# Optimization experiments

Measured on AMD Instinct MI355X. Metric: run time of the kernel, lower is better.

## Reference

```python
import jax, jax.numpy as jnp
import numpy as np

B, S, IN, D, H, FF, L = 16, 1000, 32, 512, 8, 2048, 6
DK = D // H
EPS = 1e-5


def setup_inputs() -> dict:
    key = jax.random.key(0)
    ks = iter(jax.random.split(key, 64))
    def w(shape, s=0.02):
        return jax.random.normal(next(ks), shape, dtype=jnp.float32) * s
    inp = {
        'x': jax.random.normal(next(ks), (B, S, IN), dtype=jnp.float32),
        # input projection
        'Win': w((IN, D)), 'b_in': jnp.zeros((D,), jnp.float32),
        # per-layer attention weights (stacked over L layers)
        'Wq': w((L, D, D)), 'bq': jnp.zeros((L, D), jnp.float32),
        'Wk': w((L, D, D)), 'bk': jnp.zeros((L, D), jnp.float32),
        'Wv': w((L, D, D)), 'bv': jnp.zeros((L, D), jnp.float32),
        'Wo': w((L, D, D)), 'bo': jnp.zeros((L, D), jnp.float32),
        # per-layer feed-forward
        'W1': w((L, D, FF)), 'b1': jnp.zeros((L, FF), jnp.float32),
        'W2': w((L, FF, D)), 'b2': jnp.zeros((L, D), jnp.float32),
        # per-layer layernorms
        'ln1_g': jnp.ones((L, D), jnp.float32), 'ln1_b': jnp.zeros((L, D), jnp.float32),
        'ln2_g': jnp.ones((L, D), jnp.float32), 'ln2_b': jnp.zeros((L, D), jnp.float32),
        # final encoder norm
        'lnf_g': jnp.ones((D,), jnp.float32), 'lnf_b': jnp.zeros((D,), jnp.float32),
        # feature extraction head: D -> D/2 -> D/4
        'Wf1': w((D, D // 2)), 'bf1': jnp.zeros((D // 2,), jnp.float32),
        'Wf2': w((D // 2, D // 4)), 'bf2': jnp.zeros((D // 4,), jnp.float32),
        # reconstruction head: D/4 -> D/2 -> D -> IN
        'Wr1': w((D // 4, D // 2)), 'br1': jnp.zeros((D // 2,), jnp.float32),
        'Wr2': w((D // 2, D)), 'br2': jnp.zeros((D,), jnp.float32),
        'Wr3': w((D, IN)), 'br3': jnp.zeros((IN,), jnp.float32),
        # anomaly head: D/4 -> D/8 -> 1
        'Wa1': w((D // 4, D // 8)), 'ba1': jnp.zeros((D // 8,), jnp.float32),
        'Wa2': w((D // 8, 1)), 'ba2': jnp.zeros((1,), jnp.float32),
    }
    return inp


def _layernorm(x, g, b):
    m = jnp.mean(x, axis=-1, keepdims=True)
    v = jnp.var(x, axis=-1, keepdims=True)
    return (x - m) * jax.lax.rsqrt(v + EPS) * g + b


def _pos_encoding(seq_len, d_model):
    pos = jnp.arange(seq_len, dtype=jnp.float32)[:, None]
    div = jnp.exp(jnp.arange(0, d_model, 2, dtype=jnp.float32) * (-np.log(10000.0) / d_model))
    pe = jnp.zeros((seq_len, d_model), jnp.float32)
    pe = pe.at[:, 0::2].set(jnp.sin(pos * div))
    pe = pe.at[:, 1::2].set(jnp.cos(pos * div))
    return pe


def _encoder(h, Wq, bq, Wk, bk, Wv, bv, Wo, bo, W1, b1, W2, b2,
             ln1_g, ln1_b, ln2_g, ln2_b, lnf_g, lnf_b):
    h = h + _pos_encoding(h.shape[1], D)[None]
    scale = 1.0 / np.sqrt(DK)
    for i in range(L):
        # multi-head self-attention
        q = (h @ Wq[i] + bq[i]).reshape(B, S, H, DK).transpose(0, 2, 1, 3)
        k = (h @ Wk[i] + bk[i]).reshape(B, S, H, DK).transpose(0, 2, 1, 3)
        v = (h @ Wv[i] + bv[i]).reshape(B, S, H, DK).transpose(0, 2, 1, 3)
        scores = jnp.einsum('bhsd,bhtd->bhst', q, k) * scale  # [B,H,S,S]
        attn = jax.nn.softmax(scores, axis=-1)
        ctx = jnp.einsum('bhst,bhtd->bhsd', attn, v)
        ctx = ctx.transpose(0, 2, 1, 3).reshape(B, S, D)
        attn_out = ctx @ Wo[i] + bo[i]
        h = _layernorm(h + attn_out, ln1_g[i], ln1_b[i])
        # feed-forward
        ff = jax.nn.relu(h @ W1[i] + b1[i]) @ W2[i] + b2[i]
        h = _layernorm(h + ff, ln2_g[i], ln2_b[i])
    return _layernorm(h, lnf_g, lnf_b)


def reference(x, Win, b_in, Wq, bq, Wk, bk, Wv, bv, Wo, bo, W1, b1, W2, b2,
              ln1_g, ln1_b, ln2_g, ln2_b, lnf_g, lnf_b,
              Wf1, bf1, Wf2, bf2, Wr1, br1, Wr2, br2, Wr3, br3,
              Wa1, ba1, Wa2, ba2):
    h = x @ Win + b_in  # [B,S,D]
    h = _encoder(h, Wq, bq, Wk, bk, Wv, bv, Wo, bo, W1, b1, W2, b2,
                 ln1_g, ln1_b, ln2_g, ln2_b, lnf_g, lnf_b)
    feat = jax.nn.relu(h @ Wf1 + bf1) @ Wf2 + bf2  # [B,S,D/4]
    recon = jax.nn.relu(jax.nn.relu(feat @ Wr1 + br1) @ Wr2 + br2) @ Wr3 + br3  # [B,S,IN]
    anomaly = jax.nn.sigmoid(jax.nn.relu(feat @ Wa1 + ba1) @ Wa2 + ba2)  # [B,S,1]
    return recon, anomaly
```

## Files before the change

kernel.cpp:

```cpp
#include <hip/hip_runtime.h>
#include <hip/hip_bf16.h>
#include <math.h>

#define B_  16
#define S_  1000
#define IN_ 32
#define D_  512
#define H_  8
#define FF_ 2048
#define L_  6
#define DK_ 64
#define M_  (B_ * S_)
#define SP_ 1024

typedef __bf16 bf16x8 __attribute__((ext_vector_type(8)));
typedef float  floatx4 __attribute__((ext_vector_type(4)));

#define FLAG_RELU 1
#define FLAG_BF16 2
#define FLAG_QKV  4

#define QSCALE 0.18033688011112042f

__device__ __forceinline__ void gll16(const __bf16* g, __bf16* l) {
    __builtin_amdgcn_global_load_lds(
        (const __attribute__((address_space(1))) unsigned int*)g,
        (__attribute__((address_space(3))) unsigned int*)l, 16, 0, 0);
}

__global__ __launch_bounds__(256) void gemm_mfma(
    const __bf16* __restrict__ A, const __bf16* __restrict__ BT,
    const float* __restrict__ bias, void* __restrict__ C,
    int M, int N, int K, int flags)
{
    __shared__ __bf16 Asm[128 * 32];
    __shared__ __bf16 Bsm[128 * 32];

    int tid  = threadIdx.x;
    int wave = tid >> 6;
    int lane = tid & 63;
    int bm = blockIdx.y * 128;
    int bn = blockIdx.x * 128;
    int wm = (wave & 1) * 64;
    int wn = (wave >> 1) * 64;
    int lm = lane & 15;
    int lq = lane >> 4;

    floatx4 acc[4][4] = {};

    int crow  = tid >> 2;
    int cpart = (tid & 3) * 8;
    const __bf16* ag0 = A + (size_t)(bm + crow) * K + cpart;
    const __bf16* ag1 = A + (size_t)(bm + 64 + crow) * K + cpart;
    __bf16* al0 = Asm + tid * 8;
    __bf16* al1 = Asm + 2048 + tid * 8;
    int nr0 = bn + crow, nr1 = bn + 64 + crow;
    const __bf16* bg0 = BT + (size_t)nr0 * K + cpart;
    const __bf16* bg1 = BT + (size_t)nr1 * K + cpart;
    __bf16* bl0 = Bsm + tid * 8;
    __bf16* bl1 = Bsm + 2048 + tid * 8;
    bool bv0 = nr0 < N, bv1 = nr1 < N;

    for (int k0 = 0; k0 < K; k0 += 32) {
        __syncthreads();
        gll16(ag0 + k0, al0);
        gll16(ag1 + k0, al1);
        if (bv0) gll16(bg0 + k0, bl0);
        if (bv1) gll16(bg1 + k0, bl1);
        __syncthreads();

        bf16x8 af[4], bf[4];
        #pragma unroll
        for (int i = 0; i < 4; ++i) {
            af[i] = *(const bf16x8*)&Asm[(wm + i * 16 + lm) * 32 + lq * 8];
            bf[i] = *(const bf16x8*)&Bsm[(wn + i * 16 + lm) * 32 + lq * 8];
        }
        #pragma unroll
        for (int i = 0; i < 4; ++i)
            #pragma unroll
            for (int j = 0; j < 4; ++j)
                acc[i][j] = __builtin_amdgcn_mfma_f32_16x16x32_bf16(
                    af[i], bf[j], acc[i][j], 0, 0, 0);
    }

    if (flags & FLAG_QKV) {
        int sec = bn >> 9;
        if (sec < 2) {
            __bf16* dst = (__bf16*)C + (sec ? (size_t)8192000 : 0);
            #pragma unroll
            for (int j = 0; j < 4; ++j) {
                int col = (bn & 511) + wn + j * 16 + lm;
                float bvv = bias[bn + wn + j * 16 + lm];
                #pragma unroll
                for (int i = 0; i < 4; ++i)
                    #pragma unroll
                    for (int r = 0; r < 4; ++r) {
                        int m = bm + wm + i * 16 + lq * 4 + r;
                        dst[(size_t)m * 512 + col] = (__bf16)(acc[i][j][r] + bvv);
                    }
            }
        } else {
            __bf16* vt = (__bf16*)C + (size_t)16384000;
            int bbq[4], s0[4];
            #pragma unroll
            for (int i = 0; i < 4; ++i) {
                int m0 = bm + wm + i * 16 + lq * 4;
                bbq[i] = m0 / 1000;
                s0[i]  = m0 - bbq[i] * 1000;
            }
            #pragma unroll
            for (int j = 0; j < 4; ++j) {
                int col = (bn & 511) + wn + j * 16 + lm;
                float bvv = bias[bn + wn + j * 16 + lm];
                int head = col >> 6, dk = col & 63;
                #pragma unroll
                for (int i = 0; i < 4; ++i) {
                    __bf16 t4[4];
                    #pragma unroll
                    for (int r = 0; r < 4; ++r) t4[r] = (__bf16)(acc[i][j][r] + bvv);
                    *(uint2*)(vt + ((size_t)(bbq[i] * H_ + head) * DK_ + dk) * SP_ + s0[i])
                        = *(uint2*)t4;
                }
            }
        }
        return;
    }

    #pragma unroll
    for (int j = 0; j < 4; ++j) {
        int n = bn + wn + j * 16 + lm;
        if (n >= N) continue;
        float bv = bias[n];
        #pragma unroll
        for (int i = 0; i < 4; ++i) {
            #pragma unroll
            for (int r = 0; r < 4; ++r) {
                int m = bm + wm + i * 16 + lq * 4 + r;
                float v = acc[i][j][r] + bv;
                if (flags & FLAG_RELU) v = fmaxf(v, 0.f);
                if (flags & FLAG_BF16) ((__bf16*)C)[(size_t)m * N + n] = (__bf16)v;
                else                   ((float*)C)[(size_t)m * N + n] = v;
            }
        }
    }
}

__device__ __forceinline__ void trans_tile(
    const float* __restrict__ src, __bf16* __restrict__ dst,
    int K, int N, float scale, int tx0, int ty0)
{
    __shared__ float t[32][33];
    int n0 = tx0 * 32, k0 = ty0 * 32;
    int tx = threadIdx.x & 31, ty = threadIdx.x >> 5;
    #pragma unroll
    for (int i = 0; i < 32; i += 8) {
        int k = k0 + ty + i, n = n0 + tx;
        t[ty + i][tx] = (k < K && n < N) ? src[(size_t)k * N + n] * scale : 0.f;
    }
    __syncthreads();
    #pragma unroll
    for (int i = 0; i < 32; i += 8) {
        int n = n0 + ty + i, k = k0 + tx;
        if (n < N && k < K) dst[(size_t)n * K + k] = (__bf16)t[tx][ty + i];
    }
}

__global__ __launch_bounds__(256) void transpose_qkvo(
    const float* __restrict__ Wq, const float* __restrict__ Wk,
    const float* __restrict__ Wv, const float* __restrict__ Wo,
    __bf16* __restrict__ WqkvT, __bf16* __restrict__ WoT)
{
    int l = blockIdx.z >> 2, which = blockIdx.z & 3;
    const float* src; __bf16* dst; float sc = 1.f;
    size_t so = (size_t)l * 512 * 512;
    if (which == 0)      { src = Wq + so; dst = WqkvT + (size_t)l * 1536 * 512; sc = QSCALE; }
    else if (which == 1) { src = Wk + so; dst = WqkvT + (size_t)l * 1536 * 512 + 512 * 512; }
    else if (which == 2) { src = Wv + so; dst = WqkvT + (size_t)l * 1536 * 512 + 1024 * 512; }
    else                 { src = Wo + so; dst = WoT + so; }
    trans_tile(src, dst, 512, 512, sc, blockIdx.x, blockIdx.y);
}

__global__ __launch_bounds__(256) void transpose_ffn(
    const float* __restrict__ W1, const float* __restrict__ W2,
    __bf16* __restrict__ W1T, __bf16* __restrict__ W2T)
{
    int l = blockIdx.z >> 1, which = blockIdx.z & 1;
    size_t so = (size_t)l * 512 * 2048;
    int K = which ? 2048 : 512, N = which ? 512 : 2048;
    if ((int)blockIdx.x >= N / 32 || (int)blockIdx.y >= K / 32) return;
    trans_tile((which ? W2 : W1) + so, (which ? W2T : W1T) + so,
               K, N, 1.f, blockIdx.x, blockIdx.y);
}

struct TDesc { const float* src; __bf16* dst; int K; int N; float scale; };
struct TDescArr { TDesc d[7]; };

__global__ __launch_bounds__(256) void transpose_misc(TDescArr ds)
{
    TDesc t = ds.d[blockIdx.z];
    if ((int)blockIdx.x * 32 >= t.N || (int)blockIdx.y * 32 >= t.K) return;
    trans_tile(t.src, t.dst, t.K, t.N, t.scale, blockIdx.x, blockIdx.y);
}

__global__ void cast_bf16(const float* __restrict__ src, __bf16* __restrict__ dst, int n)
{
    int i = blockIdx.x * 256 + threadIdx.x;
    if (i < n) dst[i] = (__bf16)src[i];
}

__global__ void concat_bias(const float* __restrict__ bq, const float* __restrict__ bk,
                            const float* __restrict__ bv, float* __restrict__ dst)
{
    int i = blockIdx.x * 256 + threadIdx.x;
    if (i >= L_ * 1536) return;
    int l = i / 1536, j = i - l * 1536;
    float v = (j < 512) ? bq[l * 512 + j] * QSCALE
            : (j < 1024) ? bk[l * 512 + j - 512]
                         : bv[l * 512 + j - 1024];
    dst[i] = v;
}

__global__ void add_pos_kernel(float* __restrict__ h, __bf16* __restrict__ hb)
{
    int idx = blockIdx.x * 256 + threadIdx.x;
    if (idx >= B_ * S_ * D_) return;
    int d = idx % D_;
    int s = (idx / D_) % S_;
    int two_i = d & ~1;
    float ang = (float)s * expf((float)two_i * (-9.210340371976184f / (float)D_));
    float v = h[idx] + ((d & 1) ? cosf(ang) : sinf(ang));
    h[idx] = v;
    hb[idx] = (__bf16)v;
}

#define AST 72

__global__ __launch_bounds__(256) void attn_mfma(
    const __bf16* __restrict__ q, const __bf16* __restrict__ k,
    const __bf16* __restrict__ vt, __bf16* __restrict__ ctx)
{
    const int qt = blockIdx.x, hh = blockIdx.y, bb = blockIdx.z;
    const int tid = threadIdx.x;
    const int wave = tid >> 6, lane = tid & 63;
    const int lm = lane & 15, lq = lane >> 4;

    __shared__ __bf16 Ks[64 * AST];
    __shared__ __bf16 Vt[64 * AST];

    const size_t headbase = (size_t)bb * S_ * D_ + hh * DK_;
    const __bf16* kbase  = k + headbase;
    const __bf16* vtbase = vt + (size_t)(bb * H_ + hh) * DK_ * SP_;

    bf16x8 af[2][2] = {};
    #pragma unroll
    for (int iq = 0; iq < 2; ++iq) {
        int qrow = qt * 128 + wave * 32 + iq * 16 + lm;
        if (qrow < S_) {
            const __bf16* qp = q + headbase + (size_t)qrow * D_;
            af[iq][0] = *(const bf16x8*)(qp + lq * 8);
            af[iq][1] = *(const bf16x8*)(qp + 32 + lq * 8);
        }
    }

    float lsum[2] = {};
    floatx4 oacc[2][4] = {};

    const int sr  = tid >> 3;
    const int sc8 = (tid & 7) * 8;
    const int colA = (sc8 & 32) | ((sc8 & 8) << 1) | ((sc8 & 16) >> 2);

    uint4 ku[2], vu[2];
    #pragma unroll
    for (int i = 0; i < 2; ++i) {
        int r = sr + i * 32;
        ku[i] = *(const uint4*)(kbase + (size_t)r * D_ + sc8);
        vu[i] = *(const uint4*)(vtbase + (size_t)r * SP_ + sc8);
    }

    for (int jt = 0; jt < 16; ++jt) {
        const int t0 = jt * 64;
        const bool tail = (jt == 15);

        __syncthreads();
        #pragma unroll
        for (int i = 0; i < 2; ++i) {
            int r = sr + i * 32;
            *(uint4*)&Ks[r * AST + sc8] = ku[i];
            uint2 vlo = make_uint2(vu[i].x, vu[i].y);
            uint2 vhi = make_uint2(vu[i].z, vu[i].w);
            *(uint2*)&Vt[r * AST + colA]     = vlo;
            *(uint2*)&Vt[r * AST + colA + 8] = vhi;
        }
        __syncthreads();

        if (jt < 15) {
            int t0n = t0 + 64;
            #pragma unroll
            for (int i = 0; i < 2; ++i) {
                int r = sr + i * 32;
                int trow = t0n + r;
                ku[i] = (trow < S_) ? *(const uint4*)(kbase + (size_t)trow * D_ + sc8)
                                    : make_uint4(0, 0, 0, 0);
                vu[i] = *(const uint4*)(vtbase + (size_t)r * SP_ + t0n + sc8);
            }
        }

        #pragma unroll
        for (int iq = 0; iq < 2; ++iq) {
            floatx4 sacc[4] = {};
            #pragma unroll
            for (int ks = 0; ks < 2; ++ks)
                #pragma unroll
                for (int jb = 0; jb < 4; ++jb) {
                    bf16x8 kf = *(const bf16x8*)&Ks[(jb * 16 + lm) * AST + ks * 32 + lq * 8];
                    sacc[jb] = __builtin_amdgcn_mfma_f32_16x16x32_bf16(
                        kf, af[iq][ks], sacc[jb], 0, 0, 0);
                }

            __bf16 pb[4][4];
            if (!tail) {
                #pragma unroll
                for (int jb = 0; jb < 4; ++jb)
                    #pragma unroll
                    for (int r = 0; r < 4; ++r) {
                        float p = exp2f(sacc[jb][r]);
                        lsum[iq] += p;
                        pb[jb][r] = (__bf16)p;
                    }
            } else {
                #pragma unroll
                for (int jb = 0; jb < 4; ++jb)
                    #pragma unroll
                    for (int r = 0; r < 4; ++r) {
                        bool valid = (t0 + jb * 16 + lq * 4 + r) < S_;
                        float p = valid ? exp2f(sacc[jb][r]) : 0.f;
                        lsum[iq] += p;
                        pb[jb][r] = (__bf16)p;
                    }
            }

            #pragma unroll
            for (int ks = 0; ks < 2; ++ks) {
                bf16x8 pa;
                #pragma unroll
                for (int j = 0; j < 8; ++j)
                    pa[j] = pb[2 * ks + (j >> 2)][j & 3];
                #pragma unroll
                for (int jb = 0; jb < 4; ++jb) {
                    bf16x8 bv = *(const bf16x8*)&Vt[(jb * 16 + lm) * AST + ks * 32 + lq * 8];
                    oacc[iq][jb] = __builtin_amdgcn_mfma_f32_16x16x32_bf16(
                        pa, bv, oacc[iq][jb], 0, 0, 0);
                }
            }
        }
    }

    #pragma unroll
    for (int iq = 0; iq < 2; ++iq) {
        float l = lsum[iq];
        l += __shfl_xor(l, 16, 64);
        l += __shfl_xor(l, 32, 64);
        float linv[4];
        #pragma unroll
        for (int r = 0; r < 4; ++r)
            linv[r] = 1.f / __shfl(l, lq * 4 + r, 64);
        #pragma unroll
        for (int jb = 0; jb < 4; ++jb)
            #pragma unroll
            for (int r = 0; r < 4; ++r) {
                int srow = qt * 128 + wave * 32 + iq * 16 + lq * 4 + r;
                if (srow < S_)
                    ctx[headbase + (size_t)srow * D_ + jb * 16 + lm] =
                        (__bf16)(oacc[iq][jb][r] * linv[r]);
            }
    }
}

__global__ __launch_bounds__(256) void ln_kernel(
    const float* __restrict__ x, const __bf16* __restrict__ delta,
    const float* __restrict__ g, const float* __restrict__ b,
    float* __restrict__ out, __bf16* __restrict__ outb, int has_delta)
{
    int row = blockIdx.x;
    int tid = threadIdx.x;
    __shared__ float red[256];

    const size_t base = (size_t)row * D_;
    float v0 = x[base + tid];
    float v1 = x[base + tid + 256];
    if (has_delta) {
        v0 += (float)delta[base + tid];
        v1 += (float)delta[base + tid + 256];
    }
    red[tid] = v0 + v1; __syncthreads();
    for (int o = 128; o > 0; o >>= 1) {
        if (tid < o) red[tid] += red[tid + o];
        __syncthreads();
    }
    float mean = red[0] * (1.f / D_);
    __syncthreads();
    float d0 = v0 - mean, d1 = v1 - mean;
    red[tid] = d0 * d0 + d1 * d1; __syncthreads();
    for (int o = 128; o > 0; o >>= 1) {
        if (tid < o) red[tid] += red[tid + o];
        __syncthreads();
    }
    float rstd = rsqrtf(red[0] * (1.f / D_) + 1e-5f);
    float o0 = d0 * rstd * g[tid]       + b[tid];
    float o1 = d1 * rstd * g[tid + 256] + b[tid + 256];
    out[base + tid]        = o0;
    out[base + tid + 256]  = o1;
    outb[base + tid]       = (__bf16)o0;
    outb[base + tid + 256] = (__bf16)o1;
}

__global__ __launch_bounds__(256) void a2_kernel(
    const float* __restrict__ a1, const float* __restrict__ Wa2,
    const float* __restrict__ ba2, float* __restrict__ out)
{
    int row = blockIdx.x * 4 + (threadIdx.x >> 6);
    int lane = threadIdx.x & 63;
    if (row >= M_) return;
    float p = a1[(size_t)row * 64 + lane] * Wa2[lane];
    for (int o = 32; o > 0; o >>= 1) p += __shfl_down(p, o, 64);
    if (lane == 0) out[row] = 1.f / (1.f + expf(-(p + ba2[0])));
}

extern "C" void kernel_launch(void* const* d_in, const int* in_sizes, int n_in,
                              void* d_out, int out_size, void* d_ws, size_t ws_size,
                              hipStream_t stream)
{
    const float* x     = (const float*)d_in[0];
    const float* Win   = (const float*)d_in[1];
    const float* b_in  = (const float*)d_in[2];
    const float* Wq    = (const float*)d_in[3];
    const float* bq    = (const float*)d_in[4];
    const float* Wk    = (const float*)d_in[5];
    const float* bk    = (const float*)d_in[6];
    const float* Wv    = (const float*)d_in[7];
    const float* bv    = (const float*)d_in[8];
    const float* Wo    = (const float*)d_in[9];
    const float* bo    = (const float*)d_in[10];
    const float* W1    = (const float*)d_in[11];
    const float* b1    = (const float*)d_in[12];
    const float* W2    = (const float*)d_in[13];
    const float* b2    = (const float*)d_in[14];
    const float* ln1_g = (const float*)d_in[15];
    const float* ln1_b = (const float*)d_in[16];
    const float* ln2_g = (const float*)d_in[17];
    const float* ln2_b = (const float*)d_in[18];
    const float* lnf_g = (const float*)d_in[19];
    const float* lnf_b = (const float*)d_in[20];
    const float* Wf1   = (const float*)d_in[21];
    const float* bf1   = (const float*)d_in[22];
    const float* Wf2   = (const float*)d_in[23];
    const float* bf2   = (const float*)d_in[24];
    const float* Wr1   = (const float*)d_in[25];
    const float* br1   = (const float*)d_in[26];
    const float* Wr2   = (const float*)d_in[27];
    const float* br2   = (const float*)d_in[28];
    const float* Wr3   = (const float*)d_in[29];
    const float* br3   = (const float*)d_in[30];
    const float* Wa1   = (const float*)d_in[31];
    const float* ba1   = (const float*)d_in[32];
    const float* Wa2   = (const float*)d_in[33];
    const float* ba2   = (const float*)d_in[34];

    float* recon_out   = (float*)d_out;
    float* anomaly_out = (float*)d_out + (size_t)M_ * IN_;

    char* ws = (char*)d_ws;
    float*  h    = (float*)(ws + 0);
    __bf16* tmpb = (__bf16*)(ws + 32768000);
    __bf16* hb   = (__bf16*)(ws + 65536000);
    __bf16* qb   = (__bf16*)(ws + 81920000);
    __bf16* kb   = (__bf16*)(ws + 98304000);
    __bf16* vtb  = (__bf16*)(ws + 114688000);
    __bf16* ctxb = (__bf16*)(ws + 131465216);
    __bf16* ffmid = qb;

    __bf16* t1b   = (__bf16*)(ws + 81920000);
    __bf16* featb = (__bf16*)(ws + 90112000);
    __bf16* r1b   = (__bf16*)(ws + 94208000);
    __bf16* r2b   = (__bf16*)(ws + 102400000);
    float*  a1b   = (float*)(ws + 118784000);

    size_t woff = 147849216;
    auto alloc_bf = [&](size_t elems) { __bf16* p = (__bf16*)(ws + woff); woff += elems * 2; return p; };
    __bf16* WinT  = alloc_bf(32 * 512);
    __bf16* WqkvT = alloc_bf((size_t)L_ * 1536 * 512);
    __bf16* WoT   = alloc_bf((size_t)L_ * 512 * 512);
    __bf16* W1T   = alloc_bf((size_t)L_ * 512 * 2048);
    __bf16* W2T   = alloc_bf((size_t)L_ * 2048 * 512);
    __bf16* Wf1T  = alloc_bf(512 * 256);
    __bf16* Wf2T  = alloc_bf(256 * 128);
    __bf16* Wr1T  = alloc_bf(128 * 256);
    __bf16* Wr2T  = alloc_bf(256 * 512);
    __bf16* Wr3T  = alloc_bf(512 * 32);
    __bf16* Wa1T  = alloc_bf(128 * 64);
    __bf16* xb    = alloc_bf((size_t)M_ * IN_);
    float*  bqkv  = (float*)(ws + woff);  woff += (size_t)L_ * 1536 * 4;

    dim3 blk(256);
    auto gg = [](int N) { return dim3((N + 127) / 128, M_ / 128); };

    hipLaunchKernelGGL(transpose_qkvo, dim3(16, 16, L_ * 4), blk, 0, stream,
                       Wq, Wk, Wv, Wo, WqkvT, WoT);
    hipLaunchKernelGGL(transpose_ffn, dim3(64, 64, L_ * 2), blk, 0, stream,
                       W1, W2, W1T, W2T);
    TDescArr misc;
    misc.d[0] = {Win, WinT, 32, 512, 1.f};
    misc.d[1] = {Wf1, Wf1T, 512, 256, 1.f};
    misc.d[2] = {Wf2, Wf2T, 256, 128, 1.f};
    misc.d[3] = {Wr1, Wr1T, 128, 256, 1.f};
    misc.d[4] = {Wr2, Wr2T, 256, 512, 1.f};
    misc.d[5] = {Wr3, Wr3T, 512, 32, 1.f};
    misc.d[6] = {Wa1, Wa1T, 128, 64, 1.f};
    hipLaunchKernelGGL(transpose_misc, dim3(16, 16, 7), blk, 0, stream, misc);
    hipLaunchKernelGGL(cast_bf16, dim3((M_ * IN_ + 255) / 256), blk, 0, stream,
                       x, xb, M_ * IN_);
    hipLaunchKernelGGL(concat_bias, dim3((L_ * 1536 + 255) / 256), blk, 0, stream,
                       bq, bk, bv, bqkv);

    hipLaunchKernelGGL(gemm_mfma, gg(D_), blk, 0, stream,
                       xb, WinT, b_in, (void*)h, M_, D_, IN_, 0);
    hipLaunchKernelGGL(add_pos_kernel, dim3((B_ * S_ * D_ + 255) / 256), blk, 0, stream,
                       h, hb);

    for (int l = 0; l < L_; ++l) {
        size_t wo = (size_t)l * 512 * 512;
        size_t fo = (size_t)l * 512 * 2048;

        hipLaunchKernelGGL(gemm_mfma, dim3(12, M_ / 128), blk, 0, stream,
                           hb, WqkvT + (size_t)l * 1536 * 512, bqkv + (size_t)l * 1536,
                           (void*)qb, M_, 1536, 512, FLAG_QKV);

        hipLaunchKernelGGL(attn_mfma, dim3(8, H_, B_), blk, 0, stream,
                           qb, kb, vtb, ctxb);

        hipLaunchKernelGGL(gemm_mfma, gg(D_), blk, 0, stream,
                           ctxb, WoT + wo, bo + (size_t)l * D_, (void*)tmpb, M_, D_, D_,
                           FLAG_BF16);
        hipLaunchKernelGGL(ln_kernel, dim3(M_), blk, 0, stream,
                           h, tmpb, ln1_g + (size_t)l * D_, ln1_b + (size_t)l * D_, h, hb, 1);

        hipLaunchKernelGGL(gemm_mfma, gg(FF_), blk, 0, stream,
                           hb, W1T + fo, b1 + (size_t)l * FF_, (void*)ffmid, M_, FF_, D_,
                           FLAG_RELU | FLAG_BF16);
        hipLaunchKernelGGL(gemm_mfma, gg(D_), blk, 0, stream,
                           ffmid, W2T + fo, b2 + (size_t)l * D_, (void*)tmpb, M_, D_, FF_,
                           FLAG_BF16);
        hipLaunchKernelGGL(ln_kernel, dim3(M_), blk, 0, stream,
                           h, tmpb, ln2_g + (size_t)l * D_, ln2_b + (size_t)l * D_, h, hb, 1);
    }

    hipLaunchKernelGGL(ln_kernel, dim3(M_), blk, 0, stream,
                       h, nullptr, lnf_g, lnf_b, h, hb, 0);

    hipLaunchKernelGGL(gemm_mfma, gg(256), blk, 0, stream,
                       hb, Wf1T, bf1, (void*)t1b, M_, 256, 512, FLAG_RELU | FLAG_BF16);
    hipLaunchKernelGGL(gemm_mfma, gg(128), blk, 0, stream,
                       t1b, Wf2T, bf2, (void*)featb, M_, 128, 256, FLAG_BF16);

    hipLaunchKernelGGL(gemm_mfma, gg(256), blk, 0, stream,
                       featb, Wr1T, br1, (void*)r1b, M_, 256, 128, FLAG_RELU | FLAG_BF16);
    hipLaunchKernelGGL(gemm_mfma, gg(512), blk, 0, stream,
                       r1b, Wr2T, br2, (void*)r2b, M_, 512, 256, FLAG_RELU | FLAG_BF16);
    hipLaunchKernelGGL(gemm_mfma, gg(IN_), blk, 0, stream,
                       r2b, Wr3T, br3, (void*)recon_out, M_, IN_, 512, 0);

    hipLaunchKernelGGL(gemm_mfma, gg(64), blk, 0, stream,
                       featb, Wa1T, ba1, (void*)a1b, M_, 64, 128, FLAG_RELU);
    hipLaunchKernelGGL(a2_kernel, dim3((M_ + 3) / 4), blk, 0, stream,
                       a1b, Wa2, ba2, anomaly_out);
}
```

Before: 2.015 ms.

## Load attention K/V fragments directly from global memory, dropping LDS staging

The attention kernel no longer stages K and V tiles through shared memory with barriers. Each wave now loads its MFMA fragments straight from global memory, relying on the cache for reuse across the four waves of a block. Blocks are launched on a 1D grid with a remapped index so that blocks sharing a head are spread across the chip, and s_setprio wraps the MFMA bursts. Occupancy is raised through launch bounds. This removes LDS traffic and synchronisation, but every wave now issues redundant global loads and the V loads are narrow, uncoalesced 8-byte reads.

```diff
diff --git a/kernel.cpp b/kernel.cpp
--- a/kernel.cpp
+++ b/kernel.cpp
@@ -233,19 +233,17 @@
     hb[idx] = (__bf16)v;
 }
 
-#define AST 72
-
-__global__ __launch_bounds__(256) void attn_mfma(
+__global__ __launch_bounds__(256, 4) void attn_mfma(
     const __bf16* __restrict__ q, const __bf16* __restrict__ k,
     const __bf16* __restrict__ vt, __bf16* __restrict__ ctx)
 {
-    const int qt = blockIdx.x, hh = blockIdx.y, bb = blockIdx.z;
+    const int id = blockIdx.x;
+    const int w  = (id & 7) * 128 + (id >> 3);
+    const int qt = w & 7, hh = (w >> 3) & 7, bb = w >> 6;
+
     const int tid = threadIdx.x;
     const int wave = tid >> 6, lane = tid & 63;
     const int lm = lane & 15, lq = lane >> 4;
-
-    __shared__ __bf16 Ks[64 * AST];
-    __shared__ __bf16 Vt[64 * AST];
 
     const size_t headbase = (size_t)bb * S_ * D_ + hh * DK_;
     const __bf16* kbase  = k + headbase;
@@ -265,67 +263,44 @@
     float lsum[2] = {};
     floatx4 oacc[2][4] = {};
 
-    const int sr  = tid >> 3;
-    const int sc8 = (tid & 7) * 8;
-    const int colA = (sc8 & 32) | ((sc8 & 8) << 1) | ((sc8 & 16) >> 2);
-
-    uint4 ku[2], vu[2];
-    #pragma unroll
-    for (int i = 0; i < 2; ++i) {
-        int r = sr + i * 32;
-        ku[i] = *(const uint4*)(kbase + (size_t)r * D_ + sc8);
-        vu[i] = *(const uint4*)(vtbase + (size_t)r * SP_ + sc8);
-    }
+    const __bf16* kf_p = kbase  + (size_t)lm * D_  + lq * 8;
+    const __bf16* bv_p = vtbase + (size_t)lm * SP_ + lq * 4;
 
     for (int jt = 0; jt < 16; ++jt) {
         const int t0 = jt * 64;
         const bool tail = (jt == 15);
 
-        __syncthreads();
-        #pragma unroll
-        for (int i = 0; i < 2; ++i) {
-            int r = sr + i * 32;
-            *(uint4*)&Ks[r * AST + sc8] = ku[i];
-            uint2 vlo = make_uint2(vu[i].x, vu[i].y);
-            uint2 vhi = make_uint2(vu[i].z, vu[i].w);
-            *(uint2*)&Vt[r * AST + colA]     = vlo;
-            *(uint2*)&Vt[r * AST + colA + 8] = vhi;
-        }
-        __syncthreads();
-
-        if (jt < 15) {
-            int t0n = t0 + 64;
-            #pragma unroll
-            for (int i = 0; i < 2; ++i) {
-                int r = sr + i * 32;
-                int trow = t0n + r;
-                ku[i] = (trow < S_) ? *(const uint4*)(kbase + (size_t)trow * D_ + sc8)
-                                    : make_uint4(0, 0, 0, 0);
-                vu[i] = *(const uint4*)(vtbase + (size_t)r * SP_ + t0n + sc8);
-            }
-        }
-
-        #pragma unroll
-        for (int iq = 0; iq < 2; ++iq) {
-            floatx4 sacc[4] = {};
+        bf16x8 kf[2][4];
+        #pragma unroll
+        for (int jb = 0; jb < 4; ++jb) {
+            const __bf16* kr = kf_p + (size_t)(t0 + jb * 16) * D_;
+            kf[0][jb] = *(const bf16x8*)kr;
+            kf[1][jb] = *(const bf16x8*)(kr + 32);
+        }
+
+        floatx4 sacc[2][4] = {};
+        __builtin_amdgcn_s_setprio(1);
+        #pragma unroll
+        for (int iq = 0; iq < 2; ++iq)
             #pragma unroll
             for (int ks = 0; ks < 2; ++ks)
                 #pragma unroll
-                for (int jb = 0; jb < 4; ++jb) {
-                    bf16x8 kf = *(const bf16x8*)&Ks[(jb * 16 + lm) * AST + ks * 32 + lq * 8];
-                    sacc[jb] = __builtin_amdgcn_mfma_f32_16x16x32_bf16(
-                        kf, af[iq][ks], sacc[jb], 0, 0, 0);
-                }
-
-            __bf16 pb[4][4];
+                for (int jb = 0; jb < 4; ++jb)
+                    sacc[iq][jb] = __builtin_amdgcn_mfma_f32_16x16x32_bf16(
+                        kf[ks][jb], af[iq][ks], sacc[iq][jb], 0, 0, 0);
+        __builtin_amdgcn_s_setprio(0);
+
+        bf16x8 pf[2][2];
+        #pragma unroll
+        for (int iq = 0; iq < 2; ++iq) {
             if (!tail) {
                 #pragma unroll
                 for (int jb = 0; jb < 4; ++jb)
                     #pragma unroll
                     for (int r = 0; r < 4; ++r) {
-                        float p = exp2f(sacc[jb][r]);
+                        float p = exp2f(sacc[iq][jb][r]);
                         lsum[iq] += p;
-                        pb[jb][r] = (__bf16)p;
+                        pf[iq][jb >> 1][(jb & 1) * 4 + r] = (__bf16)p;
                     }
             } else {
                 #pragma unroll
@@ -333,25 +308,33 @@
                     #pragma unroll
                     for (int r = 0; r < 4; ++r) {
                         bool valid = (t0 + jb * 16 + lq * 4 + r) < S_;
-                        float p = valid ? exp2f(sacc[jb][r]) : 0.f;
+                        float p = valid ? exp2f(sacc[iq][jb][r]) : 0.f;
                         lsum[iq] += p;
-                        pb[jb][r] = (__bf16)p;
+                        pf[iq][jb >> 1][(jb & 1) * 4 + r] = (__bf16)p;
                     }
             }
-
-            #pragma unroll
-            for (int ks = 0; ks < 2; ++ks) {
-                bf16x8 pa;
+        }
+
+        #pragma unroll
+        for (int ks = 0; ks < 2; ++ks) {
+            uint2 lo[4], hi[4];
+            #pragma unroll
+            for (int jb = 0; jb < 4; ++jb) {
+                const __bf16* vr = bv_p + (size_t)(jb * 16) * SP_ + t0 + ks * 32;
+                lo[jb] = *(const uint2*)vr;
+                hi[jb] = *(const uint2*)(vr + 16);
+            }
+            __builtin_amdgcn_s_setprio(1);
+            #pragma unroll
+            for (int jb = 0; jb < 4; ++jb) {
+                union { uint4 u; bf16x8 v; } cv;
+                cv.u = make_uint4(lo[jb].x, lo[jb].y, hi[jb].x, hi[jb].y);
                 #pragma unroll
-                for (int j = 0; j < 8; ++j)
-                    pa[j] = pb[2 * ks + (j >> 2)][j & 3];
-                #pragma unroll
-                for (int jb = 0; jb < 4; ++jb) {
-                    bf16x8 bv = *(const bf16x8*)&Vt[(jb * 16 + lm) * AST + ks * 32 + lq * 8];
+                for (int iq = 0; iq < 2; ++iq)
                     oacc[iq][jb] = __builtin_amdgcn_mfma_f32_16x16x32_bf16(
-                        pa, bv, oacc[iq][jb], 0, 0, 0);
-                }
-            }
+                        pf[iq][ks], cv.v, oacc[iq][jb], 0, 0, 0);
+            }
+            __builtin_amdgcn_s_setprio(0);
         }
     }
 
@@ -535,7 +518,7 @@
                            hb, WqkvT + (size_t)l * 1536 * 512, bqkv + (size_t)l * 1536,
                            (void*)qb, M_, 1536, 512, FLAG_QKV);
 
-        hipLaunchKernelGGL(attn_mfma, dim3(8, H_, B_), blk, 0, stream,
+        hipLaunchKernelGGL(attn_mfma, dim3(1024), blk, 0, stream,
                            qb, kb, vtb, ctxb);
 
         hipLaunchKernelGGL(gemm_mfma, gg(D_), blk, 0, stream,
```

After: 2.688 ms. 1.33x slower.

## Double-buffer attention K/V tiles, compute row sums via MFMA, remap block order

Applied to the files above, without the earlier changes.

Restructures the attention kernel to double-buffer K and V tiles in shared memory, cutting the per-tile barriers from two to one. The softmax denominator is now accumulated with an MFMA against a ones vector, replacing scalar adds and cross-lane shuffles. The launch becomes a flat 1D grid with a swizzled block-to-(tile, head, batch) mapping, and launch bounds request 4 blocks per CU. s_setprio hints are placed around the MFMA bursts. The cost is twice the shared memory, more register pressure, and row sums taken from bf16-rounded probabilities.

```diff
diff --git a/kernel.cpp b/kernel.cpp
--- a/kernel.cpp
+++ b/kernel.cpp
@@ -235,17 +235,20 @@
 
 #define AST 72
 
-__global__ __launch_bounds__(256) void attn_mfma(
+__global__ __launch_bounds__(256, 4) void attn_mfma(
     const __bf16* __restrict__ q, const __bf16* __restrict__ k,
     const __bf16* __restrict__ vt, __bf16* __restrict__ ctx)
 {
-    const int qt = blockIdx.x, hh = blockIdx.y, bb = blockIdx.z;
+    const int id = blockIdx.x;
+    const int w  = (id & 7) * 128 + (id >> 3);
+    const int qt = w & 7, hh = (w >> 3) & 7, bb = w >> 6;
+
     const int tid = threadIdx.x;
     const int wave = tid >> 6, lane = tid & 63;
     const int lm = lane & 15, lq = lane >> 4;
 
-    __shared__ __bf16 Ks[64 * AST];
-    __shared__ __bf16 Vt[64 * AST];
+    __shared__ __bf16 Ks[2][64 * AST];
+    __shared__ __bf16 Vt[2][64 * AST];
 
     const size_t headbase = (size_t)bb * S_ * D_ + hh * DK_;
     const __bf16* kbase  = k + headbase;
@@ -262,8 +265,12 @@
         }
     }
 
-    float lsum[2] = {};
     floatx4 oacc[2][4] = {};
+    floatx4 lacc[2] = {};
+
+    bf16x8 ones8;
+    #pragma unroll
+    for (int j = 0; j < 8; ++j) ones8[j] = (__bf16)1.f;
 
     const int sr  = tid >> 3;
     const int sc8 = (tid & 7) * 8;
@@ -276,80 +283,105 @@
         ku[i] = *(const uint4*)(kbase + (size_t)r * D_ + sc8);
         vu[i] = *(const uint4*)(vtbase + (size_t)r * SP_ + sc8);
     }
+    #pragma unroll
+    for (int i = 0; i < 2; ++i) {
+        int r = sr + i * 32;
+        *(uint4*)&Ks[0][r * AST + sc8] = ku[i];
+        uint2 vlo = make_uint2(vu[i].x, vu[i].y);
+        uint2 vhi = make_uint2(vu[i].z, vu[i].w);
+        *(uint2*)&Vt[0][r * AST + colA]     = vlo;
+        *(uint2*)&Vt[0][r * AST + colA + 8] = vhi;
+    }
+    __syncthreads();
+    #pragma unroll
+    for (int i = 0; i < 2; ++i) {
+        int r = sr + i * 32;
+        ku[i] = *(const uint4*)(kbase + (size_t)(64 + r) * D_ + sc8);
+        vu[i] = *(const uint4*)(vtbase + (size_t)r * SP_ + 64 + sc8);
+    }
 
     for (int jt = 0; jt < 16; ++jt) {
+        const int cur = jt & 1;
         const int t0 = jt * 64;
         const bool tail = (jt == 15);
-
-        __syncthreads();
-        #pragma unroll
-        for (int i = 0; i < 2; ++i) {
-            int r = sr + i * 32;
-            *(uint4*)&Ks[r * AST + sc8] = ku[i];
-            uint2 vlo = make_uint2(vu[i].x, vu[i].y);
-            uint2 vhi = make_uint2(vu[i].z, vu[i].w);
-            *(uint2*)&Vt[r * AST + colA]     = vlo;
-            *(uint2*)&Vt[r * AST + colA + 8] = vhi;
-        }
-        __syncthreads();
-
-        if (jt < 15) {
-            int t0n = t0 + 64;
-            #pragma unroll
-            for (int i = 0; i < 2; ++i) {
-                int r = sr + i * 32;
-                int trow = t0n + r;
-                ku[i] = (trow < S_) ? *(const uint4*)(kbase + (size_t)trow * D_ + sc8)
-                                    : make_uint4(0, 0, 0, 0);
-                vu[i] = *(const uint4*)(vtbase + (size_t)r * SP_ + t0n + sc8);
-            }
-        }
-
+        const __bf16* Kc = Ks[cur];
+        const __bf16* Vc = Vt[cur];
+
+        bf16x8 pf[2][2];
         #pragma unroll
         for (int iq = 0; iq < 2; ++iq) {
             floatx4 sacc[4] = {};
+            __builtin_amdgcn_s_setprio(1);
             #pragma unroll
             for (int ks = 0; ks < 2; ++ks)
                 #pragma unroll
                 for (int jb = 0; jb < 4; ++jb) {
-                    bf16x8 kf = *(const bf16x8*)&Ks[(jb * 16 + lm) * AST + ks * 32 + lq * 8];
+                    bf16x8 kf = *(const bf16x8*)&Kc[(jb * 16 + lm) * AST + ks * 32 + lq * 8];
                     sacc[jb] = __builtin_amdgcn_mfma_f32_16x16x32_bf16(
                         kf, af[iq][ks], sacc[jb], 0, 0, 0);
                 }
-
-            __bf16 pb[4][4];
+            __builtin_amdgcn_s_setprio(0);
+
             if (!tail) {
                 #pragma unroll
                 for (int jb = 0; jb < 4; ++jb)
                     #pragma unroll
-                    for (int r = 0; r < 4; ++r) {
-                        float p = exp2f(sacc[jb][r]);
-                        lsum[iq] += p;
-                        pb[jb][r] = (__bf16)p;
-                    }
+                    for (int r = 0; r < 4; ++r)
+                        pf[iq][jb >> 1][(jb & 1) * 4 + r] = (__bf16)exp2f(sacc[jb][r]);
             } else {
                 #pragma unroll
                 for (int jb = 0; jb < 4; ++jb)
                     #pragma unroll
                     for (int r = 0; r < 4; ++r) {
                         bool valid = (t0 + jb * 16 + lq * 4 + r) < S_;
-                        float p = valid ? exp2f(sacc[jb][r]) : 0.f;
-                        lsum[iq] += p;
-                        pb[jb][r] = (__bf16)p;
+                        pf[iq][jb >> 1][(jb & 1) * 4 + r] =
+                            valid ? (__bf16)exp2f(sacc[jb][r]) : (__bf16)0.f;
                     }
             }
-
-            #pragma unroll
-            for (int ks = 0; ks < 2; ++ks) {
-                bf16x8 pa;
+        }
+
+        #pragma unroll
+        for (int ks = 0; ks < 2; ++ks) {
+            bf16x8 bvf[4];
+            #pragma unroll
+            for (int jb = 0; jb < 4; ++jb)
+                bvf[jb] = *(const bf16x8*)&Vc[(jb * 16 + lm) * AST + ks * 32 + lq * 8];
+            __builtin_amdgcn_s_setprio(1);
+            #pragma unroll
+            for (int jb = 0; jb < 4; ++jb)
                 #pragma unroll
-                for (int j = 0; j < 8; ++j)
-                    pa[j] = pb[2 * ks + (j >> 2)][j & 3];
+                for (int iq = 0; iq < 2; ++iq)
+                    oacc[iq][jb] = __builtin_amdgcn_mfma_f32_16x16x32_bf16(
+                        pf[iq][ks], bvf[jb], oacc[iq][jb], 0, 0, 0);
+            #pragma unroll
+            for (int iq = 0; iq < 2; ++iq)
+                lacc[iq] = __builtin_amdgcn_mfma_f32_16x16x32_bf16(
+                    pf[iq][ks], ones8, lacc[iq], 0, 0, 0);
+            __builtin_amdgcn_s_setprio(0);
+        }
+
+        if (jt < 15) {
+            __bf16* Kn = Ks[cur ^ 1];
+            __bf16* Vn = Vt[cur ^ 1];
+            #pragma unroll
+            for (int i = 0; i < 2; ++i) {
+                int r = sr + i * 32;
+                *(uint4*)&Kn[r * AST + sc8] = ku[i];
+                uint2 vlo = make_uint2(vu[i].x, vu[i].y);
+                uint2 vhi = make_uint2(vu[i].z, vu[i].w);
+                *(uint2*)&Vn[r * AST + colA]     = vlo;
+                *(uint2*)&Vn[r * AST + colA + 8] = vhi;
+            }
+            __syncthreads();
+            if (jt < 14) {
+                int t0n = t0 + 128;
                 #pragma unroll
-                for (int jb = 0; jb < 4; ++jb) {
-                    bf16x8 bv = *(const bf16x8*)&Vt[(jb * 16 + lm) * AST + ks * 32 + lq * 8];
-                    oacc[iq][jb] = __builtin_amdgcn_mfma_f32_16x16x32_bf16(
-                        pa, bv, oacc[iq][jb], 0, 0, 0);
+                for (int i = 0; i < 2; ++i) {
+                    int r = sr + i * 32;
+                    int trow = t0n + r;
+                    ku[i] = (trow < S_) ? *(const uint4*)(kbase + (size_t)trow * D_ + sc8)
+                                        : make_uint4(0, 0, 0, 0);
+                    vu[i] = *(const uint4*)(vtbase + (size_t)r * SP_ + t0n + sc8);
                 }
             }
         }
@@ -357,13 +389,10 @@
 
     #pragma unroll
     for (int iq = 0; iq < 2; ++iq) {
-        float l = lsum[iq];
-        l += __shfl_xor(l, 16, 64);
-        l += __shfl_xor(l, 32, 64);
         float linv[4];
         #pragma unroll
         for (int r = 0; r < 4; ++r)
-            linv[r] = 1.f / __shfl(l, lq * 4 + r, 64);
+            linv[r] = 1.f / lacc[iq][r];
         #pragma unroll
         for (int jb = 0; jb < 4; ++jb)
             #pragma unroll
@@ -535,7 +564,7 @@
                            hb, WqkvT + (size_t)l * 1536 * 512, bqkv + (size_t)l * 1536,
                            (void*)qb, M_, 1536, 512, FLAG_QKV);
 
-        hipLaunchKernelGGL(attn_mfma, dim3(8, H_, B_), blk, 0, stream,
+        hipLaunchKernelGGL(attn_mfma, dim3(1024), blk, 0, stream,
                            qb, kb, vtb, ctxb);
 
         hipLaunchKernelGGL(gemm_mfma, gg(D_), blk, 0, stream,
```

Result: slower. 2.066 ms (+2.5%).

## Compute softmax row sums via MFMA, remap attention grid, add wave priorities

Applied to the files above, without the earlier changes.

The attention kernel now gets the softmax denominator from an extra MFMA of the bf16 probabilities against a ones vector, replacing the per-lane float sums and cross-lane shuffles. The sum therefore uses the same bf16-rounded probabilities as the P·V product. The launch changes from a 3D grid to a flat 1D grid whose block index is swizzled (id&7)*128+(id>>3), likely to spread heads and batches across XCDs for better cache locality. s_setprio is raised around the MFMA sections so waves issuing matrix work get scheduling priority. The cost is one extra MFMA per k-step.

```diff
diff --git a/kernel.cpp b/kernel.cpp
--- a/kernel.cpp
+++ b/kernel.cpp
@@ -239,7 +239,10 @@
     const __bf16* __restrict__ q, const __bf16* __restrict__ k,
     const __bf16* __restrict__ vt, __bf16* __restrict__ ctx)
 {
-    const int qt = blockIdx.x, hh = blockIdx.y, bb = blockIdx.z;
+    const int id = blockIdx.x;
+    const int w  = (id & 7) * 128 + (id >> 3);
+    const int qt = w & 7, hh = (w >> 3) & 7, bb = w >> 6;
+
     const int tid = threadIdx.x;
     const int wave = tid >> 6, lane = tid & 63;
     const int lm = lane & 15, lq = lane >> 4;
@@ -262,8 +265,12 @@
         }
     }
 
-    float lsum[2] = {};
     floatx4 oacc[2][4] = {};
+    floatx4 lacc[2] = {};
+
+    bf16x8 ones8;
+    #pragma unroll
+    for (int j = 0; j < 8; ++j) ones8[j] = (__bf16)1.f;
 
     const int sr  = tid >> 3;
     const int sc8 = (tid & 7) * 8;
@@ -308,6 +315,7 @@
         #pragma unroll
         for (int iq = 0; iq < 2; ++iq) {
             floatx4 sacc[4] = {};
+            __builtin_amdgcn_s_setprio(1);
             #pragma unroll
             for (int ks = 0; ks < 2; ++ks)
                 #pragma unroll
@@ -316,54 +324,50 @@
                     sacc[jb] = __builtin_amdgcn_mfma_f32_16x16x32_bf16(
                         kf, af[iq][ks], sacc[jb], 0, 0, 0);
                 }
-
-            __bf16 pb[4][4];
+            __builtin_amdgcn_s_setprio(0);
+
+            bf16x8 pf[2];
             if (!tail) {
                 #pragma unroll
                 for (int jb = 0; jb < 4; ++jb)
                     #pragma unroll
-                    for (int r = 0; r < 4; ++r) {
-                        float p = exp2f(sacc[jb][r]);
-                        lsum[iq] += p;
-                        pb[jb][r] = (__bf16)p;
-                    }
+                    for (int r = 0; r < 4; ++r)
+                        pf[jb >> 1][(jb & 1) * 4 + r] = (__bf16)exp2f(sacc[jb][r]);
             } else {
                 #pragma unroll
                 for (int jb = 0; jb < 4; ++jb)
                     #pragma unroll
                     for (int r = 0; r < 4; ++r) {
                         bool valid = (t0 + jb * 16 + lq * 4 + r) < S_;
-                        float p = valid ? exp2f(sacc[jb][r]) : 0.f;
-                        lsum[iq] += p;
-                        pb[jb][r] = (__bf16)p;
+                        pf[jb >> 1][(jb & 1) * 4 + r] =
+                            valid ? (__bf16)exp2f(sacc[jb][r]) : (__bf16)0.f;
                     }
             }
 
             #pragma unroll
             for (int ks = 0; ks < 2; ++ks) {
-                bf16x8 pa;
-                #pragma unroll
-                for (int j = 0; j < 8; ++j)
-                    pa[j] = pb[2 * ks + (j >> 2)][j & 3];
-                #pragma unroll
-                for (int jb = 0; jb < 4; ++jb) {
-                    bf16x8 bv = *(const bf16x8*)&Vt[(jb * 16 + lm) * AST + ks * 32 + lq * 8];
+                bf16x8 bvf[4];
+                #pragma unroll
+                for (int jb = 0; jb < 4; ++jb)
+                    bvf[jb] = *(const bf16x8*)&Vt[(jb * 16 + lm) * AST + ks * 32 + lq * 8];
+                __builtin_amdgcn_s_setprio(1);
+                #pragma unroll
+                for (int jb = 0; jb < 4; ++jb)
                     oacc[iq][jb] = __builtin_amdgcn_mfma_f32_16x16x32_bf16(
-                        pa, bv, oacc[iq][jb], 0, 0, 0);
-                }
+                        pf[ks], bvf[jb], oacc[iq][jb], 0, 0, 0);
+                lacc[iq] = __builtin_amdgcn_mfma_f32_16x16x32_bf16(
+                    pf[ks], ones8, lacc[iq], 0, 0, 0);
+                __builtin_amdgcn_s_setprio(0);
             }
         }
     }
 
     #pragma unroll
     for (int iq = 0; iq < 2; ++iq) {
-        float l = lsum[iq];
-        l += __shfl_xor(l, 16, 64);
-        l += __shfl_xor(l, 32, 64);
         float linv[4];
         #pragma unroll
         for (int r = 0; r < 4; ++r)
-            linv[r] = 1.f / __shfl(l, lq * 4 + r, 64);
+            linv[r] = 1.f / lacc[iq][r];
         #pragma unroll
         for (int jb = 0; jb < 4; ++jb)
             #pragma unroll
@@ -535,7 +539,7 @@
                            hb, WqkvT + (size_t)l * 1536 * 512, bqkv + (size_t)l * 1536,
                            (void*)qb, M_, 1536, 512, FLAG_QKV);
 
-        hipLaunchKernelGGL(attn_mfma, dim3(8, H_, B_), blk, 0, stream,
+        hipLaunchKernelGGL(attn_mfma, dim3(1024), blk, 0, stream,
                            qb, kb, vtb, ctxb);
 
         hipLaunchKernelGGL(gemm_mfma, gg(D_), blk, 0, stream,
```

New measurement: 2.010 ms. No clear change (-0.3%).
